# Kernel optimization log

Measured on AMD Instinct MI355X. Metric: run time of the kernel, lower is better.

Reference implementation:

```python
import jax, jax.numpy as jnp
import numpy as np

N, E = 20000, 320000          # nodes, edges (avg in-degree ~16)
F_IN, EMB, T, OUT = 40, 40, 5, 2
F_T = EMB // T                # per-tower output width = 8
EPS_STD, EPS_GN = 1e-5, 1e-5


def _lin_init(k, fan_in, fan_out, extra=()):
    return jax.random.normal(k, (*extra, fan_in, fan_out), jnp.float32) / np.sqrt(fan_in)


def setup_inputs() -> dict:
    key = jax.random.key(0)
    ks = jax.random.split(key, 8)
    # deg histogram in init: all 20000 nodes with degree 16 -> avg_deg['log'] = log(16+1)
    return dict(
        x=jax.random.normal(ks[0], (N, F_IN), jnp.float32),
        edge_index=jax.random.randint(ks[1], (2, E), 0, N),
        W_pre=_lin_init(ks[2], 2 * F_IN, F_IN, (T,)),   # per-tower pre-MLP
        b_pre=jnp.zeros((T, F_IN), jnp.float32),
        W_post=_lin_init(ks[3], 13 * F_IN, F_T, (T,)),  # (4 agg * 3 scalers + 1 residual) * F_in
        b_post=jnp.zeros((T, F_T), jnp.float32),
        W_lin=_lin_init(ks[4], T * F_T, EMB),           # PNAConv final mixing linear
        b_lin=jnp.zeros((EMB,), jnp.float32),
        gn_weight=jnp.ones((EMB,), jnp.float32),
        gn_bias=jnp.zeros((EMB,), jnp.float32),
        gn_mean_scale=jnp.ones((EMB,), jnp.float32),
        W1=_lin_init(ks[5], EMB, EMB),                  # head hidden linear
        b1=jnp.zeros((EMB,), jnp.float32),
        W2=_lin_init(ks[6], EMB, OUT),                  # head output linear
        b2=jnp.zeros((OUT,), jnp.float32),
        avg_deg_log=jnp.float32(np.log(17.0)),
    )


def _pna_conv(x, src, dst, W_pre, b_pre, W_post, b_post, W_lin, b_lin, avg_deg_log):
    xi, xj = x[dst], x[src]                              # gather: [E, F]
    h = jnp.concatenate([xi, xj], axis=-1)               # [E, 2F]
    m = jnp.einsum('ef,tfg->etg', h, W_pre) + b_pre      # per-tower messages [E, T, F]
    cnt = jax.ops.segment_sum(jnp.ones((E,), m.dtype), dst, num_segments=N)  # in-degree [N]
    denom = jnp.maximum(cnt, 1.0)[:, None, None]
    mean = jax.ops.segment_sum(m, dst, num_segments=N) / denom
    mean2 = jax.ops.segment_sum(m * m, dst, num_segments=N) / denom
    std = jnp.sqrt(jax.nn.relu(mean2 - mean * mean) + EPS_STD)
    has = (cnt > 0)[:, None, None]
    mn = jnp.where(has, jax.ops.segment_min(m, dst, num_segments=N), 0.0)
    mx = jnp.where(has, jax.ops.segment_max(m, dst, num_segments=N), 0.0)
    agg = jnp.concatenate([mean, mn, mx, std], axis=-1)  # [N, T, 4F]
    deg = jnp.maximum(cnt, 1.0)[:, None, None]
    logd = jnp.log(deg + 1.0)
    out = jnp.concatenate(
        [agg, agg * (logd / avg_deg_log), agg * (avg_deg_log / logd)], axis=-1)  # [N, T, 12F]
    out = jnp.concatenate(
        [jnp.broadcast_to(x[:, None, :], (N, T, x.shape[-1])), out], axis=-1)    # [N, T, 13F]
    out = jnp.einsum('ntf,tfg->ntg', out, W_post) + b_post                       # [N, T, F_T]
    return out.reshape(N, T * F_T) @ W_lin + b_lin


def _graph_norm(x, w, b, mean_scale):
    mean = jnp.mean(x, axis=0, keepdims=True)
    out = x - mean_scale * mean
    var = jnp.mean(out * out, axis=0, keepdims=True)
    return w * out / jnp.sqrt(var + EPS_GN) + b


def reference(x, edge_index, W_pre, b_pre, W_post, b_post, W_lin, b_lin,
              gn_weight, gn_bias, gn_mean_scale, W1, b1, W2, b2, avg_deg_log):
    src, dst = edge_index[0], edge_index[1]
    h = _pna_conv(x, src, dst, W_pre, b_pre, W_post, b_post, W_lin, b_lin, avg_deg_log)
    h = jax.nn.relu(_graph_norm(h, gn_weight, gn_bias, gn_mean_scale))
    h = jax.nn.relu(h @ W1 + b1)   # dropout_rate=None -> no dropout
    return h @ W2 + b2
```

## Files before the change

### kernel.cpp

```cpp
#include <hip/hip_runtime.h>
#include <math.h>

#define N_NODES 20000
#define N_EDGES 320000
#define F_IN 40
#define T_TOW 5
#define EMB 40
#define NPB 4
#define NPB_PRE 16
#define NBLK_MIX 313
#define NBLK_POST 79
#define PLANE (T_TOW * N_NODES * 40)
#define ECHUNK 16
#define STRIDE 64

typedef __attribute__((ext_vector_type(8))) _Float16 half8;

#define WS_STATS   0
#define WS_CURSOR  320
#define WS_SSRC    80384
#define WS_MS      5200384
#define WS_MD      13200384
#define WS_AGG     21200384
#define WS_XPOST   53200384
#define WS_POSTT   56400384
#define WS_H0T     69200384
#define WS_PART    72400384

__global__ __launch_bounds__(256) void k_pre(const float* __restrict__ x,
                                             const float* __restrict__ W_pre,
                                             const float* __restrict__ b_pre,
                                             const float* __restrict__ W_post,
                                             const float* __restrict__ b_post,
                                             _Float16* __restrict__ mS,
                                             _Float16* __restrict__ mD,
                                             float* __restrict__ xpostT,
                                             int* __restrict__ cursor) {
  const int tid = threadIdx.x;
  const int n0 = blockIdx.x * NPB_PRE;
  if (tid < NPB_PRE) cursor[n0 + tid] = (n0 + tid) * STRIDE;
  const bool statlane = tid < 200;
  const int q = tid - 200;
  const bool xplane = (q >= 0 && q < 40);
  const int tc = statlane ? tid : 199;
  const int t = tc / 40, g = tc - t * 40;
  const int t2 = xplane ? q / 8 : 0, g2 = xplane ? q - (q / 8) * 8 : 0;
  float wA[40], wB[40];
  const float* Wt = W_pre + t * 3200;
#pragma unroll
  for (int j = 0; j < 40; ++j) {
    wA[j] = statlane ? Wt[j * 40 + g] : W_post[t2 * 4160 + j * 8 + g2];
    wB[j] = statlane ? Wt[(40 + j) * 40 + g] : 0.f;
  }
  const float bias = statlane ? b_pre[t * 40 + g] : b_post[t2 * 8 + g2];
  for (int ni = 0; ni < NPB_PRE; ++ni) {
    const int n = n0 + ni;
    const float* xr = x + n * F_IN;
    float aA = bias, aB = 0.f;
#pragma unroll
    for (int j = 0; j < 40; j += 4) {
      const float4 xv = *(const float4*)(xr + j);
      aA += xv.x * wA[j] + xv.y * wA[j + 1] + xv.z * wA[j + 2] + xv.w * wA[j + 3];
      aB += xv.x * wB[j] + xv.y * wB[j + 1] + xv.z * wB[j + 2] + xv.w * wB[j + 3];
    }
    if (statlane) {
      mD[n * 200 + tc] = (_Float16)aA;
      mS[n * 200 + tc] = (_Float16)aB;
    } else if (xplane) {
      xpostT[t2 * (N_NODES * 8) + n * 8 + g2] = aA;
    }
  }
}

__global__ __launch_bounds__(256) void k_scatter(const int* __restrict__ src,
                                                 const int* __restrict__ dst,
                                                 int* __restrict__ cursor,
                                                 int* __restrict__ ssrc) {
  int i = blockIdx.x * 256 + threadIdx.x;
  if (i < N_EDGES) {
    int d = dst[i];
    int pos = atomicAdd(&cursor[d], 1);
    ssrc[pos] = src[i];
  }
}

__global__ __launch_bounds__(256) void k_edge(const _Float16* __restrict__ mS,
                                              const _Float16* __restrict__ mD,
                                              const int* __restrict__ cursor,
                                              const int* __restrict__ ssrc,
                                              _Float16* __restrict__ aggS) {
  const int tid = threadIdx.x;
  const int tc = tid < 200 ? tid : 199;
  const bool active = tid < 200;
  const int t = tc / 40, g = tc - t * 40;
  const int n0 = blockIdx.x * NPB;
  for (int ni = 0; ni < NPB; ++ni) {
    const int n = n0 + ni;
    const int r0 = n * STRIDE;
    const int r1 = __builtin_amdgcn_readfirstlane(cursor[n]);
    const float md = (float)mD[n * 200 + tc];
    const int cnt = r1 - r0;
    float mean, mn, mx, sd;
    if (cnt > 0) {
      float sum = 0.f, ssq = 0.f;
      mn = 3.4e38f;
      mx = -3.4e38f;
      float vlast = 0.f;
      for (int p = r0; p < r1; p += ECHUNK) {
        _Float16 h[ECHUNK];
#pragma unroll
        for (int i = 0; i < ECHUNK; ++i) {
          const int qe = (p + i < r1) ? (p + i) : (r1 - 1);
          const int s = __builtin_amdgcn_readfirstlane(ssrc[qe]);
          h[i] = mS[s * 200 + tc];
        }
#pragma unroll
        for (int i = 0; i < ECHUNK; ++i) {
          const float v = (float)h[i];
          sum += v;
          ssq = fmaf(v, v, ssq);
          mn = fminf(mn, v);
          mx = fmaxf(mx, v);
        }
        vlast = (float)h[ECHUNK - 1];
      }
      const int padded = ((cnt + ECHUNK - 1) / ECHUNK) * ECHUNK;
      const float d = (float)(padded - cnt);
      sum = fmaf(-d, vlast, sum);
      ssq = fmaf(-d, vlast * vlast, ssq);
      const float inv = 1.f / (float)cnt;
      const float ms_mean = sum * inv;
      const float var = ssq * inv - ms_mean * ms_mean;
      sd = sqrtf(fmaxf(var, 0.f) + 1e-5f);
      mean = md + ms_mean;
      mn = md + mn;
      mx = md + mx;
    } else {
      mean = 0.f; mn = 0.f; mx = 0.f; sd = sqrtf(1e-5f);
    }
    if (active) {
      _Float16* a = aggS + (t * N_NODES + n) * 40 + g;
      a[0] = (_Float16)mean;
      a[PLANE] = (_Float16)mn;
      a[2 * PLANE] = (_Float16)mx;
      a[3 * PLANE] = (_Float16)sd;
    }
  }
}

__global__ __launch_bounds__(256) void k_post(const _Float16* __restrict__ aggS,
                                              const int* __restrict__ cursor,
                                              const float* __restrict__ W_post,
                                              const float* __restrict__ avg_dl,
                                              float* __restrict__ postT4) {
  __shared__ _Float16 sAgg[256 * 42];
  const int t = blockIdx.y;
  const int s = blockIdx.z;
  const int tid = threadIdx.x;
  const int n0 = blockIdx.x * 256;
  const _Float16* gsrc = aggS + s * PLANE + (t * N_NODES + n0) * 40;
  const int lim = (N_NODES - n0) * 40;
  for (int i = 0; i < 40; ++i) {
    const int idx = tid + i * 256;
    const _Float16 vv = (idx < lim) ? gsrc[idx] : (_Float16)0.f;
    sAgg[(idx / 40) * 42 + (idx - (idx / 40) * 40)] = vv;
  }
  __syncthreads();
  const int n = n0 + tid;
  const bool ok = n < N_NODES;
  const int nn = ok ? n : N_NODES - 1;
  const int cnt = cursor[nn] - nn * STRIDE;
  const float degf = fmaxf((float)cnt, 1.f);
  const float logd = logf(degf + 1.f);
  const float avg = avg_dl[0];
  const float s1 = logd / avg, s2 = avg / logd;
  const float* Wt = W_post + t * 4160;
  float acc[8];
#pragma unroll
  for (int g2 = 0; g2 < 8; ++g2) acc[g2] = 0.f;
  const _Float16* myrow = sAgg + tid * 42;
  for (int i = 0; i < 5; ++i) {
#pragma unroll
    for (int jj = 0; jj < 8; ++jj) {
      const int kj = s * 40 + i * 8 + jj;
      const float val = (float)myrow[i * 8 + jj];
      const float* wa = Wt + (40 + kj) * 8;
      const float* wb = Wt + (200 + kj) * 8;
      const float* wc = Wt + (360 + kj) * 8;
#pragma unroll
      for (int g2 = 0; g2 < 8; ++g2)
        acc[g2] += val * (wa[g2] + s1 * wb[g2] + s2 * wc[g2]);
    }
  }
  if (ok) {
    float* pr = postT4 + ((s * T_TOW + t) * N_NODES + n) * 8;
    float4 o0 = {acc[0], acc[1], acc[2], acc[3]};
    float4 o1 = {acc[4], acc[5], acc[6], acc[7]};
    *(float4*)(pr) = o0;
    *(float4*)(pr + 4) = o1;
  }
}

__global__ __launch_bounds__(256) void k_mix(const float* __restrict__ postT4,
                                             const float* __restrict__ xpostT,
                                             const float* __restrict__ W_lin,
                                             const float* __restrict__ b_lin,
                                             float* __restrict__ h0T,
                                             float* __restrict__ partial) {
  __shared__ float sP[64 * 41];
  const int tid = threadIdx.x;
  const int n0 = blockIdx.x * 64;
  for (int i = 0; i < 10; ++i) {
    const int idx = tid + i * 256;
    const int tt = idx >> 9;
    const int r = idx & 511;
    const int row = r >> 3, c = r & 7;
    const int nn0 = n0 + row;
    const int nn = (nn0 < N_NODES) ? nn0 : 0;
    float val = xpostT[tt * (N_NODES * 8) + nn * 8 + c];
#pragma unroll
    for (int s = 0; s < 4; ++s)
      val += postT4[((s * T_TOW + tt) * N_NODES + nn) * 8 + c];
    sP[row * 41 + tt * 8 + c] = (nn0 < N_NODES) ? val : 0.f;
  }
  __syncthreads();
  const int wv = tid >> 6, lane = tid & 63;
  const int n = n0 + lane;
  const bool ok = n < N_NODES;
  for (int c = wv; c < 5; c += 4) {
    const int c0 = c * 8;
    const float4 bb0 = *(const float4*)(b_lin + c0);
    const float4 bb1 = *(const float4*)(b_lin + c0 + 4);
    float a0 = bb0.x, a1 = bb0.y, a2 = bb0.z, a3 = bb0.w;
    float a4 = bb1.x, a5 = bb1.y, a6 = bb1.z, a7 = bb1.w;
    for (int k = 0; k < 40; ++k) {
      const float p = sP[lane * 41 + k];
      const float* w = W_lin + k * EMB + c0;
      const float4 w0 = *(const float4*)(w);
      const float4 w1 = *(const float4*)(w + 4);
      a0 = fmaf(p, w0.x, a0); a1 = fmaf(p, w0.y, a1);
      a2 = fmaf(p, w0.z, a2); a3 = fmaf(p, w0.w, a3);
      a4 = fmaf(p, w1.x, a4); a5 = fmaf(p, w1.y, a5);
      a6 = fmaf(p, w1.z, a6); a7 = fmaf(p, w1.w, a7);
    }
    if (ok) {
      h0T[(c0 + 0) * N_NODES + n] = a0;
      h0T[(c0 + 1) * N_NODES + n] = a1;
      h0T[(c0 + 2) * N_NODES + n] = a2;
      h0T[(c0 + 3) * N_NODES + n] = a3;
      h0T[(c0 + 4) * N_NODES + n] = a4;
      h0T[(c0 + 5) * N_NODES + n] = a5;
      h0T[(c0 + 6) * N_NODES + n] = a6;
      h0T[(c0 + 7) * N_NODES + n] = a7;
    } else {
      a0 = a1 = a2 = a3 = a4 = a5 = a6 = a7 = 0.f;
    }
    float s[8] = {a0, a1, a2, a3, a4, a5, a6, a7};
#pragma unroll
    for (int j = 0; j < 8; ++j) {
      float sv = s[j], qv = s[j] * s[j];
#pragma unroll
      for (int m = 32; m >= 1; m >>= 1) {
        sv += __shfl_xor(sv, m, 64);
        qv += __shfl_xor(qv, m, 64);
      }
      if (lane == 0) {
        partial[blockIdx.x * 80 + c0 + j] = sv;
        partial[blockIdx.x * 80 + 40 + c0 + j] = qv;
      }
    }
  }
}

__global__ __launch_bounds__(64) void k_stats(const float* __restrict__ partial,
                                              float* __restrict__ S1,
                                              float* __restrict__ S2) {
  const int col = blockIdx.x;
  const int lane = threadIdx.x;
  float s = 0.f;
  for (int b = lane; b < NBLK_MIX; b += 64) s += partial[b * 80 + col];
#pragma unroll
  for (int m = 32; m >= 1; m >>= 1) s += __shfl_xor(s, m, 64);
  if (lane == 0) {
    if (col < 40) S1[col] = s;
    else S2[col - 40] = s;
  }
}

__global__ __launch_bounds__(256) void k_head(const float* __restrict__ h0T,
                                              const float* __restrict__ S1,
                                              const float* __restrict__ S2,
                                              const float* __restrict__ gn_w,
                                              const float* __restrict__ gn_b,
                                              const float* __restrict__ gn_ms,
                                              const float* __restrict__ W1,
                                              const float* __restrict__ b1,
                                              const float* __restrict__ W2,
                                              const float* __restrict__ b2,
                                              float* __restrict__ out) {
  __shared__ float sV[64 * 41];
  __shared__ float sH[64 * 41];
  const int tid = threadIdx.x;
  const int n0 = blockIdx.x * 64;
  const float invN = 1.f / (float)N_NODES;
  for (int i = 0; i < 10; ++i) {
    const int idx = tid + i * 256;
    const int e = idx >> 6, r = idx & 63;
    const int nn0 = n0 + r;
    const int nn = (nn0 < N_NODES) ? nn0 : 0;
    const float M = S1[e] * invN;
    const float ms = gn_ms[e];
    const float var = S2[e] * invN - ms * (2.f - ms) * M * M;
    const float sc = gn_w[e] / sqrtf(var + 1e-5f);
    const float he = h0T[e * N_NODES + nn];
    sV[r * 41 + e] = fmaxf((he - ms * M) * sc + gn_b[e], 0.f);
  }
  __syncthreads();
  const int wv = tid >> 6, lane = tid & 63;
  const int c0 = wv * 10;
  float acc[10];
#pragma unroll
  for (int j = 0; j < 10; ++j) acc[j] = b1[c0 + j];
  for (int k = 0; k < 40; ++k) {
    const float p = sV[lane * 41 + k];
    const float* w = W1 + k * EMB + c0;
#pragma unroll
    for (int j = 0; j < 10; ++j) acc[j] = fmaf(p, w[j], acc[j]);
  }
#pragma unroll
  for (int j = 0; j < 10; ++j) sH[lane * 41 + c0 + j] = fmaxf(acc[j], 0.f);
  __syncthreads();
  if (tid < 64) {
    const int n = n0 + tid;
    if (n < N_NODES) {
      float o0 = b2[0], o1 = b2[1];
      const float* hr = sH + tid * 41;
#pragma unroll
      for (int k = 0; k < 40; ++k) {
        const float r = hr[k];
        o0 = fmaf(r, W2[k * 2], o0);
        o1 = fmaf(r, W2[k * 2 + 1], o1);
      }
      out[n * 2] = o0;
      out[n * 2 + 1] = o1;
    }
  }
}

extern "C" void kernel_launch(void* const* d_in, const int* in_sizes, int n_in,
                              void* d_out, int out_size, void* d_ws, size_t ws_size,
                              hipStream_t stream) {
  const float* x      = (const float*)d_in[0];
  const int*   ei     = (const int*)d_in[1];
  const float* W_pre  = (const float*)d_in[2];
  const float* b_pre  = (const float*)d_in[3];
  const float* W_post = (const float*)d_in[4];
  const float* b_post = (const float*)d_in[5];
  const float* W_lin  = (const float*)d_in[6];
  const float* b_lin  = (const float*)d_in[7];
  const float* gn_w   = (const float*)d_in[8];
  const float* gn_b   = (const float*)d_in[9];
  const float* gn_ms  = (const float*)d_in[10];
  const float* W1     = (const float*)d_in[11];
  const float* b1     = (const float*)d_in[12];
  const float* W2     = (const float*)d_in[13];
  const float* b2     = (const float*)d_in[14];
  const float* avg_dl = (const float*)d_in[15];
  float* out = (float*)d_out;

  char* ws = (char*)d_ws;
  float* S1   = (float*)(ws + WS_STATS);
  float* S2   = S1 + 40;
  int* cursor = (int*)(ws + WS_CURSOR);
  int* ssrc   = (int*)(ws + WS_SSRC);
  _Float16* mS   = (_Float16*)(ws + WS_MS);
  _Float16* mD   = (_Float16*)(ws + WS_MD);
  _Float16* aggS = (_Float16*)(ws + WS_AGG);
  float* xpostT  = (float*)(ws + WS_XPOST);
  float* postT4  = (float*)(ws + WS_POSTT);
  float* h0T     = (float*)(ws + WS_H0T);
  float* part    = (float*)(ws + WS_PART);
  const int* e_src = ei;
  const int* e_dst = ei + N_EDGES;

  k_pre<<<N_NODES / NPB_PRE, 256, 0, stream>>>(x, W_pre, b_pre, W_post, b_post,
                                               mS, mD, xpostT, cursor);
  k_scatter<<<(N_EDGES + 255) / 256, 256, 0, stream>>>(e_src, e_dst, cursor, ssrc);
  k_edge<<<N_NODES / NPB, 256, 0, stream>>>(mS, mD, cursor, ssrc, aggS);
  k_post<<<dim3(NBLK_POST, T_TOW, 4), 256, 0, stream>>>(aggS, cursor, W_post,
                                                        avg_dl, postT4);
  k_mix<<<NBLK_MIX, 256, 0, stream>>>(postT4, xpostT, W_lin, b_lin, h0T, part);
  k_stats<<<80, 64, 0, stream>>>(part, S1, S2);
  k_head<<<NBLK_MIX, 256, 0, stream>>>(h0T, S1, S2, gn_w, gn_b, gn_ms,
                                       W1, b1, W2, b2, out);
}
```

Measured before the change: 231.5 us.

## Map one wavefront per node in edge aggregation with packed half2 math

The edge aggregation kernel now gives each 64-lane wavefront its own destination node instead of having the whole 256-thread block walk four nodes in sequence. Each lane loads and accumulates two half2 pairs, so 100 packed channels cover the 200 tower-features. Sum, sum of squares, min and max are now accumulated in packed fp16 rather than fp32. This is meant to cut idle lanes and serial node loops and to halve load instructions. The cost is lower accumulation precision: sums of squares in fp16 can lose accuracy or overflow for large degrees.

```diff
diff --git a/kernel.cpp b/kernel.cpp
--- a/kernel.cpp
+++ b/kernel.cpp
@@ -6,7 +6,6 @@
 #define F_IN 40
 #define T_TOW 5
 #define EMB 40
-#define NPB 4
 #define NPB_PRE 16
 #define NBLK_MIX 313
 #define NBLK_POST 79
@@ -15,6 +14,7 @@
 #define STRIDE 64
 
 typedef __attribute__((ext_vector_type(8))) _Float16 half8;
+typedef __attribute__((ext_vector_type(2))) _Float16 half2_t;
 
 #define WS_STATS   0
 #define WS_CURSOR  320
@@ -89,62 +89,93 @@
                                               const int* __restrict__ cursor,
                                               const int* __restrict__ ssrc,
                                               _Float16* __restrict__ aggS) {
-  const int tid = threadIdx.x;
-  const int tc = tid < 200 ? tid : 199;
-  const bool active = tid < 200;
-  const int t = tc / 40, g = tc - t * 40;
-  const int n0 = blockIdx.x * NPB;
-  for (int ni = 0; ni < NPB; ++ni) {
-    const int n = n0 + ni;
-    const int r0 = n * STRIDE;
-    const int r1 = __builtin_amdgcn_readfirstlane(cursor[n]);
-    const float md = (float)mD[n * 200 + tc];
-    const int cnt = r1 - r0;
-    float mean, mn, mx, sd;
-    if (cnt > 0) {
-      float sum = 0.f, ssq = 0.f;
-      mn = 3.4e38f;
-      mx = -3.4e38f;
-      float vlast = 0.f;
-      for (int p = r0; p < r1; p += ECHUNK) {
-        _Float16 h[ECHUNK];
-#pragma unroll
-        for (int i = 0; i < ECHUNK; ++i) {
-          const int qe = (p + i < r1) ? (p + i) : (r1 - 1);
-          const int s = __builtin_amdgcn_readfirstlane(ssrc[qe]);
-          h[i] = mS[s * 200 + tc];
-        }
-#pragma unroll
-        for (int i = 0; i < ECHUNK; ++i) {
-          const float v = (float)h[i];
-          sum += v;
-          ssq = fmaf(v, v, ssq);
-          mn = fminf(mn, v);
-          mx = fmaxf(mx, v);
-        }
-        vlast = (float)h[ECHUNK - 1];
-      }
-      const int padded = ((cnt + ECHUNK - 1) / ECHUNK) * ECHUNK;
-      const float d = (float)(padded - cnt);
-      sum = fmaf(-d, vlast, sum);
-      ssq = fmaf(-d, vlast * vlast, ssq);
-      const float inv = 1.f / (float)cnt;
-      const float ms_mean = sum * inv;
-      const float var = ssq * inv - ms_mean * ms_mean;
-      sd = sqrtf(fmaxf(var, 0.f) + 1e-5f);
-      mean = md + ms_mean;
-      mn = md + mn;
-      mx = md + mx;
-    } else {
-      mean = 0.f; mn = 0.f; mx = 0.f; sd = sqrtf(1e-5f);
-    }
-    if (active) {
-      _Float16* a = aggS + (t * N_NODES + n) * 40 + g;
-      a[0] = (_Float16)mean;
-      a[PLANE] = (_Float16)mn;
-      a[2 * PLANE] = (_Float16)mx;
-      a[3 * PLANE] = (_Float16)sd;
-    }
+  const int lane = threadIdx.x & 63;
+  const int wv = threadIdx.x >> 6;
+  const int n = blockIdx.x * 4 + wv;
+  const int r0 = n * STRIDE;
+  const int r1 = __builtin_amdgcn_readfirstlane(cursor[n]);
+  const int cnt = r1 - r0;
+  const int cpa = lane;
+  const bool bact = lane < 36;
+  const int cpb = bact ? 64 + lane : 99;
+  const half2_t mda = ((const half2_t*)(mD + n * 200))[cpa];
+  const half2_t mdb = ((const half2_t*)(mD + n * 200))[cpb];
+
+  const _Float16 HINF = (_Float16)65504.f;
+  half2_t suma = {0, 0}, ssqa = {0, 0}, sumb = {0, 0}, ssqb = {0, 0};
+  half2_t mna = {HINF, HINF}, mxa = {-HINF, -HINF};
+  half2_t mnb = {HINF, HINF}, mxb = {-HINF, -HINF};
+  half2_t va = {0, 0}, vb = {0, 0};
+
+  if (cnt > 0) {
+    for (int p = r0; p < r1; p += ECHUNK) {
+      half2_t ha[ECHUNK], hb[ECHUNK];
+#pragma unroll
+      for (int i = 0; i < ECHUNK; ++i) {
+        const int qe = (p + i < r1) ? (p + i) : (r1 - 1);
+        const int s = __builtin_amdgcn_readfirstlane(ssrc[qe]);
+        const half2_t* row = (const half2_t*)(mS + s * 200);
+        ha[i] = row[cpa];
+        hb[i] = row[cpb];
+      }
+#pragma unroll
+      for (int i = 0; i < ECHUNK; ++i) {
+        suma += ha[i];
+        ssqa += ha[i] * ha[i];
+        mna = __builtin_elementwise_min(mna, ha[i]);
+        mxa = __builtin_elementwise_max(mxa, ha[i]);
+        sumb += hb[i];
+        ssqb += hb[i] * hb[i];
+        mnb = __builtin_elementwise_min(mnb, hb[i]);
+        mxb = __builtin_elementwise_max(mxb, hb[i]);
+      }
+      va = ha[ECHUNK - 1];
+      vb = hb[ECHUNK - 1];
+    }
+  }
+
+  const int padded = ((cnt + ECHUNK - 1) / ECHUNK) * ECHUNK;
+  const float d = (float)(padded - cnt);
+  const float inv = (cnt > 0) ? 1.f / (float)cnt : 0.f;
+#pragma unroll
+  for (int set = 0; set < 2; ++set) {
+    if (set == 1 && !bact) break;
+    const int cp = set == 0 ? cpa : cpb;
+    const half2_t sum2 = set == 0 ? suma : sumb;
+    const half2_t ssq2 = set == 0 ? ssqa : ssqb;
+    const half2_t mn2 = set == 0 ? mna : mnb;
+    const half2_t mx2 = set == 0 ? mxa : mxb;
+    const half2_t vl2 = set == 0 ? va : vb;
+    const half2_t md2 = set == 0 ? mda : mdb;
+    half2_t omean, omn, omx, osd;
+#pragma unroll
+    for (int j = 0; j < 2; ++j) {
+      float mean, mnf, mxf, sd;
+      if (cnt > 0) {
+        const float vl = (float)vl2[j];
+        const float sf = (float)sum2[j] - d * vl;
+        const float qf = (float)ssq2[j] - d * vl * vl;
+        const float msm = sf * inv;
+        const float var = qf * inv - msm * msm;
+        sd = sqrtf(fmaxf(var, 0.f) + 1e-5f);
+        const float mdf = (float)md2[j];
+        mean = mdf + msm;
+        mnf = mdf + (float)mn2[j];
+        mxf = mdf + (float)mx2[j];
+      } else {
+        mean = 0.f; mnf = 0.f; mxf = 0.f; sd = sqrtf(1e-5f);
+      }
+      omean[j] = (_Float16)mean;
+      omn[j] = (_Float16)mnf;
+      omx[j] = (_Float16)mxf;
+      osd[j] = (_Float16)sd;
+    }
+    const int t = cp / 20, g = 2 * (cp - t * 20);
+    half2_t* a = (half2_t*)(aggS + (t * N_NODES + n) * 40 + g);
+    a[0] = omean;
+    *(half2_t*)((_Float16*)a + PLANE) = omn;
+    *(half2_t*)((_Float16*)a + 2 * PLANE) = omx;
+    *(half2_t*)((_Float16*)a + 3 * PLANE) = osd;
   }
 }
 
@@ -386,7 +417,7 @@
   k_pre<<<N_NODES / NPB_PRE, 256, 0, stream>>>(x, W_pre, b_pre, W_post, b_post,
                                                mS, mD, xpostT, cursor);
   k_scatter<<<(N_EDGES + 255) / 256, 256, 0, stream>>>(e_src, e_dst, cursor, ssrc);
-  k_edge<<<N_NODES / NPB, 256, 0, stream>>>(mS, mD, cursor, ssrc, aggS);
+  k_edge<<<N_NODES / 4, 256, 0, stream>>>(mS, mD, cursor, ssrc, aggS);
   k_post<<<dim3(NBLK_POST, T_TOW, 4), 256, 0, stream>>>(aggS, cursor, W_post,
                                                         avg_dl, postT4);
   k_mix<<<NBLK_MIX, 256, 0, stream>>>(postT4, xpostT, W_lin, b_lin, h0T, part);
```

Result: faster. 220.5 us (median of 2 runs) (-4.8%).
